# Performance work log

Hardware: AMD Instinct MI355X
Metric: run time of the kernel (lower is better)

## Reference

```python
import jax, jax.numpy as jnp
import numpy as np

N_NODES = 100000
N_EDGES = 800000
F_IN, N_HID, N_CLS = 256, 128, 40


def setup_inputs() -> dict:
    key = jax.random.key(0)
    ks = jax.random.split(key, 6)
    features = jax.random.normal(ks[0], (N_NODES, F_IN), dtype=jnp.float32)
    src = jax.random.randint(ks[1], (N_EDGES,), 0, N_NODES, dtype=jnp.int64)
    dst = jax.random.randint(ks[2], (N_EDGES,), 0, N_NODES, dtype=jnp.int64)
    W1 = jax.random.normal(ks[3], (F_IN, N_HID), dtype=jnp.float32) / np.sqrt(F_IN)
    b1 = jnp.zeros((N_HID,), dtype=jnp.float32)
    W2 = jax.random.normal(ks[4], (N_HID, N_CLS), dtype=jnp.float32) / np.sqrt(N_HID)
    b2 = jnp.zeros((N_CLS,), dtype=jnp.float32)
    return {"features": features, "src": src, "dst": dst,
            "W1": W1, "b1": b1, "W2": W2, "b2": b2}


def reference(features, src, dst, W1, b1, W2, b2):
    # DGL GraphConv with norm='both': h = D_dst^{-1/2} A (D_src^{-1/2} x) W + b
    # Eval mode: dropout(p=0.85) is identity.
    N = features.shape[0]
    ones = jnp.ones(src.shape[0], dtype=features.dtype)
    out_deg = jax.ops.segment_sum(ones, src, num_segments=N)
    in_deg = jax.ops.segment_sum(ones, dst, num_segments=N)
    norm_src = jnp.where(out_deg > 0, out_deg ** -0.5, 0.0)[:, None]  # [N,1]
    norm_dst = jnp.where(in_deg > 0, in_deg ** -0.5, 0.0)[:, None]

    def gconv(x, W, b):
        # project first (in_feats >= out_feats here) to shrink SpMM width
        h = (x * norm_src) @ W                                # [N, out]
        agg = jax.ops.segment_sum(h[src], dst, num_segments=N)  # sparse aggregate
        return agg * norm_dst + b

    x = jax.nn.relu(gconv(features, W1, b1))
    return gconv(x, W2, b2)
```

## Files before the change

kernel.cpp:

```cpp
#include <hip/hip_runtime.h>
#include <hip/hip_bf16.h>
#include <math.h>


#define F_IN  256
#define F_HID 128
#define F_CLS 40

#define RSZ 8192
#define NSL 32

typedef __bf16 bf16_t;
typedef bf16_t bf16x8 __attribute__((ext_vector_type(8)));
typedef float floatx4 __attribute__((ext_vector_type(4)));
typedef _Float16 f16x8 __attribute__((ext_vector_type(8)));

static __device__ __forceinline__ unsigned short f2b(float f) {
    __hip_bfloat16 h = __float2bfloat16(f);
    return __builtin_bit_cast(unsigned short, h);
}
static __device__ __forceinline__ float b2f(unsigned short u) {
    return __uint_as_float((unsigned)u << 16);
}
static __device__ __forceinline__ unsigned short f2h(float f) {
    return __builtin_bit_cast(unsigned short, (_Float16)f);
}
static __device__ __forceinline__ float h2f(unsigned short u) {
    return (float)__builtin_bit_cast(_Float16, u);
}

__global__ __launch_bounds__(256) void hist_kernel(
    const int* __restrict__ src, const int* __restrict__ dst,
    unsigned* __restrict__ partial_s, unsigned* __restrict__ partial_d, int E)
{
    __shared__ unsigned h[RSZ];
    const int t = threadIdx.x;
    const int r  = blockIdx.x / NSL;
    const int sl = blockIdx.x % NSL;
    const int lo = r * RSZ;
    const int* __restrict__ keys = blockIdx.y ? dst : src;
    unsigned* __restrict__ part = blockIdx.y ? partial_d : partial_s;

    for (int i = t; i < RSZ; i += 256) h[i] = 0;
    __syncthreads();

    const int slice = (E + NSL - 1) / NSL;
    const int e0 = sl * slice;
    const int e1 = min(E, e0 + slice);

    int e = e0 + t;
    for (; e + 7 * 256 < e1; e += 8 * 256) {
        int k[8];
        #pragma unroll
        for (int i = 0; i < 8; ++i) k[i] = keys[e + i * 256];
        #pragma unroll
        for (int i = 0; i < 8; ++i) {
            unsigned kk = (unsigned)(k[i] - lo);
            if (kk < RSZ) atomicAdd(&h[kk], 1u);
        }
    }
    for (; e < e1; e += 256) {
        unsigned kk = (unsigned)(keys[e] - lo);
        if (kk < RSZ) atomicAdd(&h[kk], 1u);
    }
    __syncthreads();

    unsigned* dst_p = part + (size_t)blockIdx.x * RSZ;
    for (int i = t; i < RSZ; i += 256) dst_p[i] = h[i];
}

__global__ __launch_bounds__(256) void scan1_kernel(
    const unsigned* __restrict__ partial_s, const unsigned* __restrict__ partial_d,
    int* __restrict__ row_off, int* __restrict__ blk_sums,
    float* __restrict__ norm_src, float* __restrict__ norm_dst, int N)
{
    __shared__ int s[256];
    const int t = threadIdx.x;
    const int base = blockIdx.x * 1024 + t * 4;

    unsigned ss0 = 0, ss1 = 0, ss2 = 0, ss3 = 0;
    unsigned sd0 = 0, sd1 = 0, sd2 = 0, sd3 = 0;
    {
        const int r = base / RSZ;
        const int off = base & (RSZ - 1);
        const unsigned* ps = partial_s + (size_t)r * NSL * RSZ + off;
        const unsigned* pd = partial_d + (size_t)r * NSL * RSZ + off;
        #pragma unroll
        for (int sl = 0; sl < NSL; ++sl) {
            uint4 a = *(const uint4*)(ps + (size_t)sl * RSZ);
            uint4 b = *(const uint4*)(pd + (size_t)sl * RSZ);
            ss0 += a.x; ss1 += a.y; ss2 += a.z; ss3 += a.w;
            sd0 += b.x; sd1 += b.y; sd2 += b.z; sd3 += b.w;
        }
    }
    if (base + 0 < N) {
        norm_src[base + 0] = ss0 ? 1.0f / sqrtf((float)ss0) : 0.0f;
        norm_dst[base + 0] = sd0 ? 1.0f / sqrtf((float)sd0) : 0.0f;
    }
    if (base + 1 < N) {
        norm_src[base + 1] = ss1 ? 1.0f / sqrtf((float)ss1) : 0.0f;
        norm_dst[base + 1] = sd1 ? 1.0f / sqrtf((float)sd1) : 0.0f;
    }
    if (base + 2 < N) {
        norm_src[base + 2] = ss2 ? 1.0f / sqrtf((float)ss2) : 0.0f;
        norm_dst[base + 2] = sd2 ? 1.0f / sqrtf((float)sd2) : 0.0f;
    }
    if (base + 3 < N) {
        norm_src[base + 3] = ss3 ? 1.0f / sqrtf((float)ss3) : 0.0f;
        norm_dst[base + 3] = sd3 ? 1.0f / sqrtf((float)sd3) : 0.0f;
    }

    int v0 = (base + 0 < N) ? (int)sd0 : 0;
    int v1 = (base + 1 < N) ? (int)sd1 : 0;
    int v2 = (base + 2 < N) ? (int)sd2 : 0;
    int v3 = (base + 3 < N) ? (int)sd3 : 0;
    int local = v0 + v1 + v2 + v3;
    s[t] = local;
    __syncthreads();
    for (int off = 1; off < 256; off <<= 1) {
        int x = (t >= off) ? s[t - off] : 0;
        __syncthreads();
        s[t] += x;
        __syncthreads();
    }
    int excl = s[t] - local;
    if (t == 255) blk_sums[blockIdx.x] = s[t];
    if (base + 0 < N) row_off[base + 0] = excl;
    if (base + 1 < N) row_off[base + 1] = excl + v0;
    if (base + 2 < N) row_off[base + 2] = excl + v0 + v1;
    if (base + 3 < N) row_off[base + 3] = excl + v0 + v1 + v2;
}

__global__ __launch_bounds__(256) void scan2_pack_kernel(
    int* __restrict__ blk_sums, int B,
    const float* __restrict__ W1, __hip_bfloat16* __restrict__ W1t,
    const float* __restrict__ W2, unsigned short* __restrict__ W2t)
{
    const int t = threadIdx.x;
    if (blockIdx.x > 128) {
        int idx = (blockIdx.x - 129) * 256 + t;
        int n = idx >> 7;
        int k = idx & 127;
        W2t[idx] = (n < F_CLS) ? f2h(W2[(size_t)k * F_CLS + n]) : (unsigned short)0;
        return;
    }
    if (blockIdx.x > 0) {
        int idx = (blockIdx.x - 1) * 256 + t;
        int n = idx >> 8;
        int k = idx & 255;
        W1t[idx] = __float2bfloat16(W1[(size_t)k * F_HID + n]);
        return;
    }
    __shared__ int s[256];
    int local = (t < B) ? blk_sums[t] : 0;
    s[t] = local;
    __syncthreads();
    for (int off = 1; off < 256; off <<= 1) {
        int x = (t >= off) ? s[t - off] : 0;
        __syncthreads();
        s[t] += x;
        __syncthreads();
    }
    if (t < B) blk_sums[t] = s[t] - local;
}

__global__ __launch_bounds__(256) void scan3_slicepref_kernel(
    int* __restrict__ row_off, const int* __restrict__ blk_sums,
    unsigned* __restrict__ partial_d, int N, int E, int NRtot)
{
    const int idx = blockIdx.x * 256 + threadIdx.x;
    if (idx >= NRtot) return;
    unsigned run = 0;
    if (idx < N) {
        int v = row_off[idx] + blk_sums[idx >> 10];
        row_off[idx] = v;
        run = (unsigned)v;
    }
    if (idx == N) row_off[N] = E;
    const int r = idx / RSZ;
    const int i = idx & (RSZ - 1);
    unsigned* p = partial_d + (size_t)r * NSL * RSZ + i;
    #pragma unroll
    for (int sl = 0; sl < NSL; ++sl) {
        unsigned c = p[(size_t)sl * RSZ];
        p[(size_t)sl * RSZ] = run;
        run += c;
    }
}

__global__ __launch_bounds__(256) void scatter2_kernel(
    const int* __restrict__ src, const int* __restrict__ dst,
    const unsigned* __restrict__ pref, int* __restrict__ csr_src, int E)
{
    __shared__ unsigned cur[RSZ];
    const int t = threadIdx.x;
    const int r  = blockIdx.x / NSL;
    const int sl = blockIdx.x % NSL;
    const int lo = r * RSZ;
    const unsigned* p = pref + (size_t)blockIdx.x * RSZ;

    for (int i = t; i < RSZ; i += 256) cur[i] = p[i];
    __syncthreads();

    const int slice = (E + NSL - 1) / NSL;
    const int e0 = sl * slice;
    const int e1 = min(E, e0 + slice);

    int e = e0 + t;
    for (; e + 7 * 256 < e1; e += 8 * 256) {
        int d[8], s[8];
        #pragma unroll
        for (int i = 0; i < 8; ++i) { d[i] = dst[e + i * 256]; s[i] = src[e + i * 256]; }
        #pragma unroll
        for (int i = 0; i < 8; ++i) {
            unsigned k = (unsigned)(d[i] - lo);
            if (k < RSZ) {
                unsigned pos = atomicAdd(&cur[k], 1u);
                csr_src[pos] = s[i];
            }
        }
    }
    for (; e < e1; e += 256) {
        unsigned k = (unsigned)(dst[e] - lo);
        if (k < RSZ) {
            unsigned pos = atomicAdd(&cur[k], 1u);
            csr_src[pos] = src[e];
        }
    }
}

__global__ __launch_bounds__(512, 4) void gemm1_mfma_kernel(
    const float* __restrict__ X, const __hip_bfloat16* __restrict__ W1t,
    const float* __restrict__ norm_src, __hip_bfloat16* __restrict__ h1b, int N)
{
    __shared__ __hip_bfloat16 Bs[128 * 256];
    const int t = threadIdx.x;
    const int node0 = blockIdx.x * 128;
    const int lane = t & 63;
    const int w = t >> 6;
    const int l15 = lane & 15;
    const int quad = lane >> 4;

    const int arow = node0 + w * 16 + l15;
    const bool valid = arow < N;
    const int arow_c = valid ? arow : (N - 1);
    const float ns = valid ? norm_src[arow] : 0.0f;

    const float* xp = X + (size_t)arow_c * F_IN + quad * 8;

    float4 araw[4];
    araw[0] = *(const float4*)(xp + 0);
    araw[1] = *(const float4*)(xp + 4);
    araw[2] = *(const float4*)(xp + 32);
    araw[3] = *(const float4*)(xp + 36);

    #pragma unroll
    for (int i = 0; i < 8; ++i) {
        int idx = i * 512 + t;
        int row = idx >> 5;
        int ch  = idx & 31;
        uint4 v = *(const uint4*)(W1t + (size_t)row * F_IN + ch * 8);
        int d = row * 256 + ((ch * 8) ^ ((row & 7) << 3));
        *(uint4*)(Bs + d) = v;
    }
    __syncthreads();

    const int swz = (l15 & 7) << 3;
    const int bbase0 = l15 * 256 + ((quad * 8) ^ swz);
    const int bbase1 = l15 * 256 + ((32 + quad * 8) ^ swz);

    floatx4 acc[8] = {};

    #pragma unroll
    for (int c = 0; c < 4; ++c) {
        bf16x8 ab0, ab1;
        {
            union { bf16x8 v; unsigned short u[8]; } cv;
            cv.u[0] = f2b(araw[0].x * ns); cv.u[1] = f2b(araw[0].y * ns);
            cv.u[2] = f2b(araw[0].z * ns); cv.u[3] = f2b(araw[0].w * ns);
            cv.u[4] = f2b(araw[1].x * ns); cv.u[5] = f2b(araw[1].y * ns);
            cv.u[6] = f2b(araw[1].z * ns); cv.u[7] = f2b(araw[1].w * ns);
            ab0 = cv.v;
            cv.u[0] = f2b(araw[2].x * ns); cv.u[1] = f2b(araw[2].y * ns);
            cv.u[2] = f2b(araw[2].z * ns); cv.u[3] = f2b(araw[2].w * ns);
            cv.u[4] = f2b(araw[3].x * ns); cv.u[5] = f2b(araw[3].y * ns);
            cv.u[6] = f2b(araw[3].z * ns); cv.u[7] = f2b(araw[3].w * ns);
            ab1 = cv.v;
        }
        if (c < 3) {
            araw[0] = *(const float4*)(xp + (c + 1) * 64 + 0);
            araw[1] = *(const float4*)(xp + (c + 1) * 64 + 4);
            araw[2] = *(const float4*)(xp + (c + 1) * 64 + 32);
            araw[3] = *(const float4*)(xp + (c + 1) * 64 + 36);
        }
        #pragma unroll
        for (int nt = 0; nt < 8; ++nt) {
            bf16x8 b = *(const bf16x8*)(Bs + bbase0 + nt * 16 * 256 + c * 64);
            acc[nt] = __builtin_amdgcn_mfma_f32_16x16x32_bf16(ab0, b, acc[nt], 0, 0, 0);
        }
        #pragma unroll
        for (int nt = 0; nt < 8; ++nt) {
            bf16x8 b = *(const bf16x8*)(Bs + bbase1 + nt * 16 * 256 + c * 64);
            acc[nt] = __builtin_amdgcn_mfma_f32_16x16x32_bf16(ab1, b, acc[nt], 0, 0, 0);
        }
    }

    #pragma unroll
    for (int nt = 0; nt < 8; ++nt) {
        #pragma unroll
        for (int r = 0; r < 4; ++r) {
            int node = node0 + w * 16 + quad * 4 + r;
            if (node < N)
                h1b[(size_t)node * F_HID + nt * 16 + l15] = __float2bfloat16(acc[nt][r]);
        }
    }
}

__global__ __launch_bounds__(512) void spmm1_fused_kernel(
    const __hip_bfloat16* __restrict__ h1b, const int* __restrict__ row_off,
    const int* __restrict__ csr_src, const float* __restrict__ norm_src,
    const float* __restrict__ norm_dst, const float* __restrict__ b1,
    const unsigned short* __restrict__ W2t, unsigned short* __restrict__ h2, int N)
{
    __shared__ unsigned short As[16][136];
    const int t = threadIdx.x;
    const int g = t >> 5;
    const int node = blockIdx.x * 16 + g;
    const int c = (t & 31) << 2;

    if (node < N) {
        const int start = row_off[node];
        const int end = row_off[node + 1];
        float4 acc = make_float4(0.f, 0.f, 0.f, 0.f);
        int j = start;
        for (; j + 8 <= end; j += 8) {
            int s[8];
            #pragma unroll
            for (int i = 0; i < 8; ++i) s[i] = csr_src[j + i];
            ushort4 u[8];
            #pragma unroll
            for (int i = 0; i < 8; ++i)
                u[i] = *(const ushort4*)(h1b + (size_t)s[i] * F_HID + c);
            #pragma unroll
            for (int i = 0; i < 8; ++i) {
                acc.x += b2f(u[i].x);
                acc.y += b2f(u[i].y);
                acc.z += b2f(u[i].z);
                acc.w += b2f(u[i].w);
            }
        }
        for (; j + 2 <= end; j += 2) {
            int s0 = csr_src[j + 0];
            int s1 = csr_src[j + 1];
            ushort4 u0 = *(const ushort4*)(h1b + (size_t)s0 * F_HID + c);
            ushort4 u1 = *(const ushort4*)(h1b + (size_t)s1 * F_HID + c);
            acc.x += b2f(u0.x) + b2f(u1.x);
            acc.y += b2f(u0.y) + b2f(u1.y);
            acc.z += b2f(u0.z) + b2f(u1.z);
            acc.w += b2f(u0.w) + b2f(u1.w);
        }
        if (j < end) {
            int s = csr_src[j];
            ushort4 u = *(const ushort4*)(h1b + (size_t)s * F_HID + c);
            acc.x += b2f(u.x);
            acc.y += b2f(u.y);
            acc.z += b2f(u.z);
            acc.w += b2f(u.w);
        }
        const float nd = norm_dst[node];
        const float ns = norm_src[node];
        float4 bb = *(const float4*)(b1 + c);
        ushort4 o;
        o.x = f2h(fmaxf(fmaf(acc.x, nd, bb.x), 0.f) * ns);
        o.y = f2h(fmaxf(fmaf(acc.y, nd, bb.y), 0.f) * ns);
        o.z = f2h(fmaxf(fmaf(acc.z, nd, bb.z), 0.f) * ns);
        o.w = f2h(fmaxf(fmaf(acc.w, nd, bb.w), 0.f) * ns);
        *(ushort4*)&As[g][c] = o;
    } else {
        ushort4 z = make_ushort4(0, 0, 0, 0);
        *(ushort4*)&As[g][c] = z;
    }
    __syncthreads();
    if (t >= 64) return;

    const int l15 = t & 15;
    const int quad = t >> 4;
    floatx4 co[3] = {};
    #pragma unroll
    for (int kc = 0; kc < 4; ++kc) {
        f16x8 a = *(const f16x8*)&As[l15][kc * 32 + quad * 8];
        #pragma unroll
        for (int ct = 0; ct < 3; ++ct) {
            f16x8 b = *(const f16x8*)(W2t + (size_t)(ct * 16 + l15) * F_HID
                                          + kc * 32 + quad * 8);
            co[ct] = __builtin_amdgcn_mfma_f32_16x16x32_f16(a, b, co[ct], 0, 0, 0);
        }
    }
    const int node0 = blockIdx.x * 16;
    #pragma unroll
    for (int ct = 0; ct < 3; ++ct) {
        int col = ct * 16 + l15;
        if (col < F_CLS) {
            #pragma unroll
            for (int i = 0; i < 4; ++i) {
                int n2 = node0 + quad * 4 + i;
                if (n2 < N) h2[(size_t)n2 * F_CLS + col] = f2h(co[ct][i]);
            }
        }
    }
}

__global__ __launch_bounds__(256) void spmm2_csr_kernel(
    const unsigned short* __restrict__ h2, const int* __restrict__ row_off,
    const int* __restrict__ csr_src, const float* __restrict__ norm_dst,
    const float* __restrict__ b2, float* __restrict__ out, int N)
{
    const int t = threadIdx.x;
    if (t >= 250) return;
    const int node = blockIdx.x * 25 + t / 10;
    const int lane = t % 10;
    if (node >= N) return;
    const int c = lane << 2;
    const int start = row_off[node];
    const int end = row_off[node + 1];
    float4 acc = make_float4(0.f, 0.f, 0.f, 0.f);
    int j = start;
    for (; j + 8 <= end; j += 8) {
        int s[8];
        #pragma unroll
        for (int i = 0; i < 8; ++i) s[i] = csr_src[j + i];
        ushort4 u[8];
        #pragma unroll
        for (int i = 0; i < 8; ++i)
            u[i] = *(const ushort4*)(h2 + (size_t)s[i] * F_CLS + c);
        #pragma unroll
        for (int i = 0; i < 8; ++i) {
            acc.x += h2f(u[i].x);
            acc.y += h2f(u[i].y);
            acc.z += h2f(u[i].z);
            acc.w += h2f(u[i].w);
        }
    }
    for (; j + 2 <= end; j += 2) {
        int s0 = csr_src[j + 0];
        int s1 = csr_src[j + 1];
        ushort4 u0 = *(const ushort4*)(h2 + (size_t)s0 * F_CLS + c);
        ushort4 u1 = *(const ushort4*)(h2 + (size_t)s1 * F_CLS + c);
        acc.x += h2f(u0.x) + h2f(u1.x);
        acc.y += h2f(u0.y) + h2f(u1.y);
        acc.z += h2f(u0.z) + h2f(u1.z);
        acc.w += h2f(u0.w) + h2f(u1.w);
    }
    if (j < end) {
        int s = csr_src[j];
        ushort4 u = *(const ushort4*)(h2 + (size_t)s * F_CLS + c);
        acc.x += h2f(u.x);
        acc.y += h2f(u.y);
        acc.z += h2f(u.z);
        acc.w += h2f(u.w);
    }
    float nd = norm_dst[node];
    float4 bb = *(const float4*)(b2 + c);
    float4 r;
    r.x = fmaf(acc.x, nd, bb.x);
    r.y = fmaf(acc.y, nd, bb.y);
    r.z = fmaf(acc.z, nd, bb.z);
    r.w = fmaf(acc.w, nd, bb.w);
    *(float4*)(out + (size_t)node * F_CLS + c) = r;
}

extern "C" void kernel_launch(void* const* d_in, const int* in_sizes, int n_in,
                              void* d_out, int out_size, void* d_ws, size_t ws_size,
                              hipStream_t stream) {
    const float* X   = (const float*)d_in[0];
    const int*   src = (const int*)d_in[1];
    const int*   dst = (const int*)d_in[2];
    const float* W1  = (const float*)d_in[3];
    const float* b1  = (const float*)d_in[4];
    const float* W2  = (const float*)d_in[5];
    const float* b2  = (const float*)d_in[6];
    float* out = (float*)d_out;

    const int N = in_sizes[0] / F_IN;
    const int E = in_sizes[1];
    const int NB = (N + 1023) / 1024;
    const int NR = (N + RSZ - 1) / RSZ;
    const int NRtot = NR * RSZ;

    char* w = (char*)d_ws;
    int*   row_off  = (int*)w;                      w += (size_t)(N + 4) * 4;
    int*   blk_sums = (int*)w;                      w += 256 * 4;
    int*   csr_src  = (int*)w;                      w += (size_t)E * 4;
    float* norm_src = (float*)w;                    w += (size_t)N * 4;
    float* norm_dst = (float*)w;                    w += (size_t)N * 4;
    unsigned short* h2 = (unsigned short*)w;        w += (size_t)N * F_CLS * 2;
    __hip_bfloat16* W1t = (__hip_bfloat16*)w;       w += (size_t)F_HID * F_IN * 2;
    unsigned short* W2t = (unsigned short*)w;       w += (size_t)48 * F_HID * 2;
    __hip_bfloat16* h1b = (__hip_bfloat16*)w;       w += (size_t)N * F_HID * 2;
    unsigned* partial_s = (unsigned*)w;             w += (size_t)NR * NSL * RSZ * 4;
    unsigned* partial_d = (unsigned*)w;             w += (size_t)NR * NSL * RSZ * 4;

    hist_kernel<<<dim3(NR * NSL, 2), 256, 0, stream>>>(src, dst, partial_s, partial_d, E);

    scan1_kernel<<<NB, 256, 0, stream>>>(partial_s, partial_d, row_off, blk_sums,
                                         norm_src, norm_dst, N);
    scan2_pack_kernel<<<153, 256, 0, stream>>>(blk_sums, NB, W1, W1t, W2, W2t);
    scan3_slicepref_kernel<<<(NRtot + 255) / 256, 256, 0, stream>>>(
        row_off, blk_sums, partial_d, N, E, NRtot);

    scatter2_kernel<<<NR * NSL, 256, 0, stream>>>(src, dst, partial_d, csr_src, E);

    gemm1_mfma_kernel<<<(N + 127) / 128, 512, 0, stream>>>(X, W1t, norm_src, h1b, N);

    spmm1_fused_kernel<<<(N + 15) / 16, 512, 0, stream>>>(h1b, row_off, csr_src,
                                                          norm_src, norm_dst, b1,
                                                          W2t, h2, N);

    spmm2_csr_kernel<<<(N + 24) / 25, 256, 0, stream>>>(h2, row_off, csr_src,
                                                        norm_dst, b2, out, N);
}
```

Baseline: 301.7 us.

## Restructure GEMM1 to register-resident W1 fragments with 16-node blocks

GEMM1 no longer stages all of W1 into a 64 KB shared-memory tile. Each block now handles 16 nodes with 4 waves, and each wave holds its 32-column slice of W1 in registers loaded straight from global memory. The source-norm scaling moves from the input conversion to the output epilogue. This removes the LDS fill, the barrier and the LDS reads, and allows far more blocks. In exchange every block re-reads its W1 slice from global/L2, each X row is read once per wave (four times per block), and register pressure rises.

```diff
diff --git a/kernel.cpp b/kernel.cpp
--- a/kernel.cpp
+++ b/kernel.cpp
@@ -229,23 +229,19 @@
     }
 }
 
-__global__ __launch_bounds__(512, 4) void gemm1_mfma_kernel(
+__global__ __launch_bounds__(256, 4) void gemm1_mfma_kernel(
     const float* __restrict__ X, const __hip_bfloat16* __restrict__ W1t,
     const float* __restrict__ norm_src, __hip_bfloat16* __restrict__ h1b, int N)
 {
-    __shared__ __hip_bfloat16 Bs[128 * 256];
-    const int t = threadIdx.x;
-    const int node0 = blockIdx.x * 128;
+    const int t = threadIdx.x;
+    const int node0 = blockIdx.x * 16;
+    const int w = t >> 6;
     const int lane = t & 63;
-    const int w = t >> 6;
     const int l15 = lane & 15;
     const int quad = lane >> 4;
 
-    const int arow = node0 + w * 16 + l15;
-    const bool valid = arow < N;
-    const int arow_c = valid ? arow : (N - 1);
-    const float ns = valid ? norm_src[arow] : 0.0f;
-
+    const int arow = node0 + l15;
+    const int arow_c = (arow < N) ? arow : (N - 1);
     const float* xp = X + (size_t)arow_c * F_IN + quad * 8;
 
     float4 araw[4];
@@ -254,37 +250,35 @@
     araw[2] = *(const float4*)(xp + 32);
     araw[3] = *(const float4*)(xp + 36);
 
+    bf16x8 bfr[2][4][2];
     #pragma unroll
-    for (int i = 0; i < 8; ++i) {
-        int idx = i * 512 + t;
-        int row = idx >> 5;
-        int ch  = idx & 31;
-        uint4 v = *(const uint4*)(W1t + (size_t)row * F_IN + ch * 8);
-        int d = row * 256 + ((ch * 8) ^ ((row & 7) << 3));
-        *(uint4*)(Bs + d) = v;
-    }
-    __syncthreads();
-
-    const int swz = (l15 & 7) << 3;
-    const int bbase0 = l15 * 256 + ((quad * 8) ^ swz);
-    const int bbase1 = l15 * 256 + ((32 + quad * 8) ^ swz);
-
-    floatx4 acc[8] = {};
+    for (int nt = 0; nt < 2; ++nt) {
+        const __hip_bfloat16* bp = W1t + (size_t)((w * 2 + nt) * 16 + l15) * F_IN
+                                       + quad * 8;
+        #pragma unroll
+        for (int c = 0; c < 4; ++c) {
+            #pragma unroll
+            for (int h = 0; h < 2; ++h)
+                bfr[nt][c][h] = *(const bf16x8*)(bp + c * 64 + h * 32);
+        }
+    }
+
+    floatx4 acc[2] = {};
 
     #pragma unroll
     for (int c = 0; c < 4; ++c) {
         bf16x8 ab0, ab1;
         {
             union { bf16x8 v; unsigned short u[8]; } cv;
-            cv.u[0] = f2b(araw[0].x * ns); cv.u[1] = f2b(araw[0].y * ns);
-            cv.u[2] = f2b(araw[0].z * ns); cv.u[3] = f2b(araw[0].w * ns);
-            cv.u[4] = f2b(araw[1].x * ns); cv.u[5] = f2b(araw[1].y * ns);
-            cv.u[6] = f2b(araw[1].z * ns); cv.u[7] = f2b(araw[1].w * ns);
+            cv.u[0] = f2b(araw[0].x); cv.u[1] = f2b(araw[0].y);
+            cv.u[2] = f2b(araw[0].z); cv.u[3] = f2b(araw[0].w);
+            cv.u[4] = f2b(araw[1].x); cv.u[5] = f2b(araw[1].y);
+            cv.u[6] = f2b(araw[1].z); cv.u[7] = f2b(araw[1].w);
             ab0 = cv.v;
-            cv.u[0] = f2b(araw[2].x * ns); cv.u[1] = f2b(araw[2].y * ns);
-            cv.u[2] = f2b(araw[2].z * ns); cv.u[3] = f2b(araw[2].w * ns);
-            cv.u[4] = f2b(araw[3].x * ns); cv.u[5] = f2b(araw[3].y * ns);
-            cv.u[6] = f2b(araw[3].z * ns); cv.u[7] = f2b(araw[3].w * ns);
+            cv.u[0] = f2b(araw[2].x); cv.u[1] = f2b(araw[2].y);
+            cv.u[2] = f2b(araw[2].z); cv.u[3] = f2b(araw[2].w);
+            cv.u[4] = f2b(araw[3].x); cv.u[5] = f2b(araw[3].y);
+            cv.u[6] = f2b(araw[3].z); cv.u[7] = f2b(araw[3].w);
             ab1 = cv.v;
         }
         if (c < 3) {
@@ -294,24 +288,24 @@
             araw[3] = *(const float4*)(xp + (c + 1) * 64 + 36);
         }
         #pragma unroll
-        for (int nt = 0; nt < 8; ++nt) {
-            bf16x8 b = *(const bf16x8*)(Bs + bbase0 + nt * 16 * 256 + c * 64);
-            acc[nt] = __builtin_amdgcn_mfma_f32_16x16x32_bf16(ab0, b, acc[nt], 0, 0, 0);
-        }
-        #pragma unroll
-        for (int nt = 0; nt < 8; ++nt) {
-            bf16x8 b = *(const bf16x8*)(Bs + bbase1 + nt * 16 * 256 + c * 64);
-            acc[nt] = __builtin_amdgcn_mfma_f32_16x16x32_bf16(ab1, b, acc[nt], 0, 0, 0);
+        for (int nt = 0; nt < 2; ++nt) {
+            acc[nt] = __builtin_amdgcn_mfma_f32_16x16x32_bf16(ab0, bfr[nt][c][0],
+                                                              acc[nt], 0, 0, 0);
+            acc[nt] = __builtin_amdgcn_mfma_f32_16x16x32_bf16(ab1, bfr[nt][c][1],
+                                                              acc[nt], 0, 0, 0);
         }
     }
 
     #pragma unroll
-    for (int nt = 0; nt < 8; ++nt) {
-        #pragma unroll
-        for (int r = 0; r < 4; ++r) {
-            int node = node0 + w * 16 + quad * 4 + r;
-            if (node < N)
-                h1b[(size_t)node * F_HID + nt * 16 + l15] = __float2bfloat16(acc[nt][r]);
+    for (int r = 0; r < 4; ++r) {
+        int node = node0 + quad * 4 + r;
+        if (node < N) {
+            float ns = norm_src[node];
+            #pragma unroll
+            for (int nt = 0; nt < 2; ++nt) {
+                int col = (w * 2 + nt) * 16 + l15;
+                h1b[(size_t)node * F_HID + col] = __float2bfloat16(acc[nt][r] * ns);
+            }
         }
     }
 }
@@ -510,7 +504,7 @@
 
     scatter2_kernel<<<NR * NSL, 256, 0, stream>>>(src, dst, partial_d, csr_src, E);
 
-    gemm1_mfma_kernel<<<(N + 127) / 128, 512, 0, stream>>>(X, W1t, norm_src, h1b, N);
+    gemm1_mfma_kernel<<<(N + 15) / 16, 256, 0, stream>>>(X, W1t, norm_src, h1b, N);
 
     spmm1_fused_kernel<<<(N + 15) / 16, 512, 0, stream>>>(h1b, row_off, csr_src,
                                                           norm_src, norm_dst, b1,
```

Result: slower. 362.6 us (+20.2%).
